# Kernel optimization log

Hardware: AMD Instinct MI355X
Metric: run time of the kernel (lower is better)

The kernel has to match this reference:

```python
import jax, jax.numpy as jnp
import numpy as np

DEPTH_BINS = 64
TEMPERATURE = 1.0


def _conv2d(x, w, b, pad):
    y = jax.lax.conv_general_dilated(x, w, (1, 1), [(pad, pad), (pad, pad)],
                                     dimension_numbers=('NCHW', 'OIHW', 'NCHW'))
    return y + b[None, :, None, None]


def _conv3d(x, w, b, pad):
    y = jax.lax.conv_general_dilated(x, w, (1, 1, 1), [(pad, pad)] * 3,
                                     dimension_numbers=('NCDHW', 'OIDHW', 'NCDHW'))
    return y + b[None, :, None, None, None]


def setup_inputs() -> dict:
    key = jax.random.key(0)
    ks = jax.random.split(key, 16)
    B, N, C, H, W = 2, 5, 256, 96, 96
    s = 0.05  # weight scale
    return {
        'focal_features': jax.random.normal(ks[0], (B, N, C, H, W), jnp.float32),
        'focus_distances': jax.random.uniform(ks[1], (B, N), jnp.float32, 0.5, 5.0),
        'camera_encoding': jax.random.normal(ks[2], (B, 16), jnp.float32),
        'W1': jax.random.normal(ks[3], (256, 512, 3, 3), jnp.float32) * s,
        'b1': jnp.zeros((256,), jnp.float32),
        'W2': jax.random.normal(ks[4], (128, 256, 3, 3), jnp.float32) * s,
        'b2': jnp.zeros((128,), jnp.float32),
        'W3': jax.random.normal(ks[5], (1, 128, 1, 1), jnp.float32) * s,
        'b3': jnp.zeros((1,), jnp.float32),
        'R1': jax.random.normal(ks[6], (32, 64, 3, 3, 3), jnp.float32) * s,
        'rb1': jnp.zeros((32,), jnp.float32),
        'R2': jax.random.normal(ks[7], (16, 32, 3, 3, 3), jnp.float32) * s,
        'rb2': jnp.zeros((16,), jnp.float32),
        'R3': jax.random.normal(ks[8], (64, 16, 1, 1, 1), jnp.float32) * s,
        'rb3': jnp.zeros((64,), jnp.float32),
    }


def reference(focal_features, focus_distances, camera_encoding,
              W1, b1, W2, b2, W3, b3, R1, rb1, R2, rb2, R3, rb3):
    B, N, C, H, W = focal_features.shape
    # _apply_blur is identity and depth only affects the (unused) blur sigma,
    # so the per-depth matching cost is identical across all depth bins.
    feat_ref = focal_features[:, 0]  # [B,C,H,W]
    pair = jnp.concatenate(
        [focal_features, jnp.broadcast_to(feat_ref[:, None], focal_features.shape)],
        axis=2)  # [B,N,2C,H,W]
    x = pair.reshape(B * N, 2 * C, H, W)
    x = jax.nn.relu(_conv2d(x, W1, b1, 1))
    x = jax.nn.relu(_conv2d(x, W2, b2, 1))
    cost = _conv2d(x, W3, b3, 0)  # [B*N,1,H,W]
    cost_agg = cost.reshape(B, N, H, W).mean(axis=1)  # [B,H,W]
    # identical for every depth bin -> broadcast
    cv = jnp.broadcast_to(cost_agg[:, None], (B, DEPTH_BINS, H, W))
    # refine_net: Conv3d over channels=depth_bins, spatial dims (H, W, 1)
    v = cv[..., None]  # [B, depth_bins, H, W, 1]
    v = jax.nn.relu(_conv3d(v, R1, rb1, 1))
    v = jax.nn.relu(_conv3d(v, R2, rb2, 1))
    v = _conv3d(v, R3, rb3, 0)  # [B, depth_bins, H, W, 1]
    cv_ref = v[..., 0]  # [B, depth_bins, H, W]
    depth_probs = jax.nn.softmax(-cv_ref / TEMPERATURE, axis=1)
    cost_volume = jnp.transpose(cv_ref, (0, 2, 3, 1))   # [B,H,W,depth_bins]
    depth_probs = jnp.transpose(depth_probs, (0, 2, 3, 1))
    return cost_volume, depth_probs
```

## Files before the change

kernel.cpp:

```cpp
#include <hip/hip_runtime.h>
#include <stdint.h>

typedef unsigned short u16;
typedef _Float16 f16;
typedef _Float16 f16x8 __attribute__((ext_vector_type(8)));
typedef float    f32x4 __attribute__((ext_vector_type(4)));

#define HW   96
#define NPIX (HW*HW)
#define BBATCH 2
#define NVIEW  5
#define NIMG 10

#define LDS_B_OFF 6272
#define LDS_BYTES (6272 + 24576)

__device__ __forceinline__ int swz(int row, int chunk) {
    return ((row >> 1) << 7) + (((((row & 1) << 2) | chunk) ^ ((row >> 1) & 7)) << 4);
}

__device__ __forceinline__ u16 f16u(float f) {
    union { u16 u; f16 h; } v; v.h = (f16)f; return v.u;
}

__global__ __launch_bounds__(256)
void k_prep_w(const float* __restrict__ W1, const float* __restrict__ W2,
              const float* __restrict__ R1, const float* __restrict__ R2, const float* __restrict__ R3,
              u16* __restrict__ w1a, u16* __restrict__ w1b, u16* __restrict__ w2t,
              float* __restrict__ s1t, float* __restrict__ s2t, float* __restrict__ r3t)
{
    int id = blockIdx.x * 256 + threadIdx.x;
    if (id < 589824) {
        int t = id >> 16; int r = id & 65535; int o = r >> 8; int c = r & 255;
        int kh = t / 3, kw = t % 3;
        *(f16*)&w1a[id] = (f16)W1[((size_t)(o * 512 + c) * 3 + kh) * 3 + kw];
        *(f16*)&w1b[id] = (f16)W1[((size_t)(o * 512 + 256 + c) * 3 + kh) * 3 + kw];
        return;
    }
    id -= 589824;
    if (id < 294912) {
        int t = id >> 15; int r = id & 32767; int o = r >> 8; int c = r & 255;
        *(f16*)&w2t[id] = (f16)W2[((size_t)(o * 256 + c) * 3 + t / 3) * 3 + (t % 3)];
        return;
    }
    id -= 294912;
    if (id < 288) {
        int t = id >> 5; int o = id & 31;
        float s = 0.f;
        for (int i = 0; i < 64; ++i)
            s += R1[((size_t)((o * 64 + i) * 3 + t / 3) * 3 + t % 3) * 3 + 1];
        s1t[id] = s;
        return;
    }
    id -= 288;
    if (id < 4608) {
        int o = id & 15; int r = id >> 4; int i = r & 31; int t = r >> 5;
        s2t[id] = R2[((size_t)((o * 32 + i) * 3 + t / 3) * 3 + t % 3) * 3 + 1];
        return;
    }
    id -= 4608;
    if (id < 1024) {
        int o = id & 63; int i = id >> 6;
        r3t[id] = R3[(size_t)o * 16 + i];
    }
}

__global__ __launch_bounds__(256)
void k_tr(const float* __restrict__ src, u16* __restrict__ dst, int img0, int imgMul)
{
    const int cblk = blockIdx.x, row = blockIdx.y, z = blockIdx.z;
    const int gimg = img0 + z * imgMul;
    const int tid = threadIdx.x;
    __shared__ u16 tile[96 * 40];
    const int c = tid >> 3, j = tid & 7;
    const float* s = src + ((size_t)(gimg * 256 + cblk * 32 + c)) * NPIX + (size_t)row * HW + j * 12;
    #pragma unroll
    for (int k = 0; k < 3; ++k) {
        const float4 v = ((const float4*)s)[k];
        const int px = j * 12 + k * 4;
        tile[(px + 0) * 40 + c] = f16u(v.x);
        tile[(px + 1) * 40 + c] = f16u(v.y);
        tile[(px + 2) * 40 + c] = f16u(v.z);
        tile[(px + 3) * 40 + c] = f16u(v.w);
    }
    __syncthreads();
    if (tid < 192) {
        const int px = tid >> 1, part = tid & 1;
        const uint4 v0 = ((const uint4*)(tile + px * 40 + part * 16))[0];
        const uint4 v1 = ((const uint4*)(tile + px * 40 + part * 16))[1];
        uint4* d = (uint4*)(dst + ((((size_t)z * HW + row) * 8 + cblk) * HW + px) * 32 + part * 16);
        d[0] = v0; d[1] = v1;
    }
}

template<int MODE>
__global__ __launch_bounds__(256, 4)
void k_conv(const u16* __restrict__ in, const u16* __restrict__ wt,
            const u16* __restrict__ refp, const float* __restrict__ bias,
            const float* __restrict__ W3, void* __restrict__ outp, int ib)
{
    constexpr int Cout = (MODE == 2) ? 128 : 256;
    const int h  = blockIdx.x;
    const int y  = blockIdx.y;
    const int ob = blockIdx.z * 128;
    const int tid = threadIdx.x;
    const int wv = tid >> 6, l = tid & 63;
    const int wm = wv >> 1, wn = wv & 1;
    const int lane16 = l & 15, quad = l >> 4;

    __shared__ __align__(16) char lds[LDS_BYTES];

    f32x4 acc[3][4];
    #pragma unroll
    for (int mf = 0; mf < 3; ++mf)
        #pragma unroll
        for (int nf = 0; nf < 4; ++nf) acc[mf][nf] = (f32x4){0.f, 0.f, 0.f, 0.f};

    if (tid < 32) {
        const int base = (tid & 16) ? (48 * 128 + 64) : 0;
        ((unsigned int*)(lds + base))[tid & 15] = 0u;
    }

    for (int dh = -1; dh <= 1; ++dh) {
        const int hh = h + dh;
        if ((unsigned)hh >= (unsigned)HW) continue;
        for (int c0 = 0; c0 < 256; c0 += 32) {
            __syncthreads();
            if (tid < 192) {
                const int px = tid >> 1, half = tid & 1;
                const uint4* g = (const uint4*)(in +
                    ((((size_t)y * HW + hh) * 8 + (c0 >> 5)) * HW + px) * 32 + half * 16);
                const uint4 v0 = g[0], v1 = g[1];
                *(uint4*)(lds + swz(px + 1, half * 2))     = v0;
                *(uint4*)(lds + swz(px + 1, half * 2 + 1)) = v1;
            }
            #pragma unroll
            for (int i = 0; i < 3; ++i) {
                const int idx = i * 256 + tid;
                const int dwt = idx >> 8, o = (idx >> 1) & 127, half = idx & 1;
                const int tap = (dh + 1) * 3 + dwt;
                const uint4* g = (const uint4*)(wt +
                    ((size_t)tap * Cout + ob + o) * 256 + c0 + half * 16);
                const uint4 v0 = g[0], v1 = g[1];
                const int row = dwt * 128 + o;
                *(uint4*)(lds + LDS_B_OFF + swz(row, half * 2))     = v0;
                *(uint4*)(lds + LDS_B_OFF + swz(row, half * 2 + 1)) = v1;
            }
            __syncthreads();
            #pragma unroll
            for (int dw = 0; dw < 3; ++dw) {
                f16x8 af[3];
                #pragma unroll
                for (int mf = 0; mf < 3; ++mf)
                    af[mf] = *(const f16x8*)(lds + swz(wm * 48 + mf * 16 + lane16 + dw, quad));
                #pragma unroll
                for (int nf = 0; nf < 4; ++nf) {
                    const f16x8 bf = *(const f16x8*)(lds + LDS_B_OFF +
                        swz(dw * 128 + wn * 64 + nf * 16 + lane16, quad));
                    #pragma unroll
                    for (int mf = 0; mf < 3; ++mf)
                        acc[mf][nf] = __builtin_amdgcn_mfma_f32_16x16x32_f16(af[mf], bf, acc[mf][nf], 0, 0, 0);
                }
            }
        }
    }

    if (MODE <= 1) {
        const int rimg = (MODE == 1) ? (ib + y) / NVIEW : 0;
        float bias4[4] = {0.f, 0.f, 0.f, 0.f};
        if (MODE == 1) {
            #pragma unroll
            for (int nf = 0; nf < 4; ++nf) bias4[nf] = bias[ob + wn * 64 + nf * 16 + lane16];
        }
        char* epi = lds + wv * 3072;
        u16* outg = (u16*)outp;
        #pragma unroll
        for (int p = 0; p < 2; ++p) {
            __syncthreads();
            #pragma unroll
            for (int nn = 0; nn < 2; ++nn) {
                const int nf = p * 2 + nn;
                #pragma unroll
                for (int mf = 0; mf < 3; ++mf)
                    #pragma unroll
                    for (int r = 0; r < 4; ++r) {
                        const int pxl = mf * 16 + quad * 4 + r;
                        *(u16*)(epi + pxl * 64 + (nn * 16 + lane16) * 2) =
                            f16u(acc[mf][nf][r] + bias4[nf]);
                    }
            }
            __syncthreads();
            const int cblk = (ob + wn * 64 + p * 32) >> 5;
            const size_t obase = (((size_t)y * HW + h) * 8 + cblk) * (size_t)(HW * 32);
            const size_t rbase = (((size_t)rimg * HW + h) * 8 + cblk) * (size_t)(HW * 32);
            #pragma unroll
            for (int i = 0; i < 3; ++i) {
                const int u = i * 64 + l;
                const int pxl = u >> 2, part = u & 3;
                f16x8 v = *(const f16x8*)(epi + pxl * 64 + part * 16);
                const int px = wm * 48 + pxl;
                if (MODE == 1) {
                    const f16x8 rv = *(const f16x8*)(refp + rbase + (size_t)px * 32 + part * 8);
                    #pragma unroll
                    for (int jj = 0; jj < 8; ++jj)
                        v[jj] = (f16)fmaxf((float)v[jj] + (float)rv[jj], 0.f);
                }
                *(f16x8*)(outg + obase + (size_t)px * 32 + part * 8) = v;
            }
        }
    } else {
        const int gimg = ib + y;
        float w3v[4], b2v[4];
        #pragma unroll
        for (int nf = 0; nf < 4; ++nf) {
            const int o = wn * 64 + nf * 16 + lane16;
            w3v[nf] = W3[o]; b2v[nf] = bias[o];
        }
        float s[3][4];
        #pragma unroll
        for (int mf = 0; mf < 3; ++mf)
            #pragma unroll
            for (int r = 0; r < 4; ++r) {
                float t = 0.f;
                #pragma unroll
                for (int nf = 0; nf < 4; ++nf)
                    t += w3v[nf] * fmaxf(acc[mf][nf][r] + b2v[nf], 0.f);
                s[mf][r] = t;
            }
        #pragma unroll
        for (int xb = 1; xb < 16; xb <<= 1)
            #pragma unroll
            for (int mf = 0; mf < 3; ++mf)
                #pragma unroll
                for (int r = 0; r < 4; ++r)
                    s[mf][r] += __shfl_xor(s[mf][r], xb);
        __syncthreads();
        float* cs = (float*)lds;
        if (wn == 0 && lane16 == 0) {
            #pragma unroll
            for (int mf = 0; mf < 3; ++mf)
                #pragma unroll
                for (int r = 0; r < 4; ++r)
                    cs[wm * 48 + mf * 16 + quad * 4 + r] = s[mf][r];
        }
        __syncthreads();
        if (wn == 1 && lane16 == 0) {
            float* pvp = (float*)outp + (size_t)gimg * NPIX + (size_t)h * HW;
            #pragma unroll
            for (int mf = 0; mf < 3; ++mf)
                #pragma unroll
                for (int r = 0; r < 4; ++r) {
                    const int px = wm * 48 + mf * 16 + quad * 4 + r;
                    pvp[px] = cs[px] + s[mf][r];
                }
        }
    }
}

__global__ __launch_bounds__(256)
void k_cost_sum(const float* __restrict__ pv, const float* __restrict__ b3, float* __restrict__ ca)
{
    const int id = blockIdx.x * 256 + threadIdx.x;
    if (id >= BBATCH * NPIX) return;
    const int b = id / NPIX, hw = id % NPIX;
    float s = 0.f;
    #pragma unroll
    for (int n = 0; n < NVIEW; ++n) s += pv[(size_t)(b * NVIEW + n) * NPIX + hw];
    ca[id] = b3[0] + 0.2f * s;
}

__global__ __launch_bounds__(256)
void k_d1(const float* __restrict__ cost_agg, const float* __restrict__ s1t,
          const float* __restrict__ rb1, float* __restrict__ t1)
{
    const int id = blockIdx.x * 256 + threadIdx.x;
    const int o = id & 31; const int r = id >> 5;
    const int hw = r % NPIX; const int bimg = r / NPIX;
    const int y = hw / HW, x = hw % HW;
    const float* ca = cost_agg + (size_t)bimg * NPIX;
    float s = rb1[o];
    #pragma unroll
    for (int t = 0; t < 9; ++t) {
        const int yy = y + t / 3 - 1, xx = x + t % 3 - 1;
        if ((unsigned)yy < HW && (unsigned)xx < HW)
            s += s1t[t * 32 + o] * ca[yy * HW + xx];
    }
    t1[id] = fmaxf(s, 0.f);
}

__global__ __launch_bounds__(256)
void k_d2(const float* __restrict__ t1, const float* __restrict__ s2t,
          const float* __restrict__ rb2, float* __restrict__ t2)
{
    const int id = blockIdx.x * 256 + threadIdx.x;
    const int o = id & 15; const int r = id >> 4;
    const int hw = r % NPIX; const int bimg = r / NPIX;
    const int y = hw / HW, x = hw % HW;
    float s = rb2[o];
    for (int t = 0; t < 9; ++t) {
        const int yy = y + t / 3 - 1, xx = x + t % 3 - 1;
        if ((unsigned)yy < HW && (unsigned)xx < HW) {
            const float* tp = t1 + ((size_t)bimg * NPIX + yy * HW + xx) * 32;
            #pragma unroll
            for (int i = 0; i < 32; ++i)
                s += s2t[(t * 32 + i) * 16 + o] * tp[i];
        }
    }
    t2[id] = fmaxf(s, 0.f);
}

__global__ __launch_bounds__(256)
void k_d3(const float* __restrict__ t2, const float* __restrict__ r3t,
          const float* __restrict__ rb3, float* __restrict__ out)
{
    const int wv = threadIdx.x >> 6, o = threadIdx.x & 63;
    const int pix = blockIdx.x * 4 + wv;
    const float* tp = t2 + (size_t)pix * 16;
    float cv = rb3[o];
    #pragma unroll
    for (int i = 0; i < 16; ++i) cv += r3t[i * 64 + o] * tp[i];
    const float z = -cv;
    float m = z;
    #pragma unroll
    for (int off = 32; off; off >>= 1) m = fmaxf(m, __shfl_xor(m, off));
    const float e = __expf(z - m);
    float s = e;
    #pragma unroll
    for (int off = 32; off; off >>= 1) s += __shfl_xor(s, off);
    const float p = e / s;
    const size_t idx = (size_t)pix * 64 + o;
    out[idx] = cv;
    out[idx + (size_t)BBATCH * NPIX * 64] = p;
}

extern "C" void kernel_launch(void* const* d_in, const int* in_sizes, int n_in,
                              void* d_out, int out_size, void* d_ws, size_t ws_size,
                              hipStream_t stream)
{
    (void)in_sizes; (void)n_in; (void)out_size;
    const float* focal = (const float*)d_in[0];
    const float* W1  = (const float*)d_in[3];
    const float* b1  = (const float*)d_in[4];
    const float* W2  = (const float*)d_in[5];
    const float* b2  = (const float*)d_in[6];
    const float* W3  = (const float*)d_in[7];
    const float* b3  = (const float*)d_in[8];
    const float* R1  = (const float*)d_in[9];
    const float* rb1 = (const float*)d_in[10];
    const float* R2  = (const float*)d_in[11];
    const float* rb2 = (const float*)d_in[12];
    const float* R3  = (const float*)d_in[13];
    const float* rb3 = (const float*)d_in[14];

    char* ws = (char*)d_ws;
    size_t off = 0;
    auto alloc = [&](size_t sz) { char* p = ws + off; off = (off + sz + 255) & ~(size_t)255; return p; };
    const size_t IMG = (size_t)HW * 8 * HW * 32 * 2;
    u16*   w1a  = (u16*)  alloc(1179648);
    u16*   w1b  = (u16*)  alloc(1179648);
    u16*   w2t  = (u16*)  alloc(589824);
    float* s1t  = (float*)alloc(1152);
    float* s2t  = (float*)alloc(18432);
    float* r3t  = (float*)alloc(4096);
    float* ca   = (float*)alloc(73728);
    float* t1   = (float*)alloc(2359296);
    float* t2   = (float*)alloc(1179648);
    float* pv   = (float*)alloc(NIMG * NPIX * 4);
    u16*   refp   = (u16*)alloc(BBATCH * IMG);
    u16*   feats2 = (u16*)alloc(BBATCH * IMG);
    const size_t base = off;
    int C = 1;
    if (base + 20 * IMG + 512 <= ws_size)      C = 10;
    else if (base + 10 * IMG + 512 <= ws_size) C = 5;
    else if (base + 4 * IMG + 512 <= ws_size)  C = 2;
    u16* feats = (u16*)alloc((size_t)C * IMG);
    u16* x1    = (u16*)alloc((size_t)C * IMG);

    k_prep_w<<<(890656 + 255) / 256, 256, 0, stream>>>(W1, W2, R1, R2, R3, w1a, w1b, w2t, s1t, s2t, r3t);

    k_tr<<<dim3(8, HW, BBATCH), 256, 0, stream>>>(focal, feats2, 0, NVIEW);
    k_conv<0><<<dim3(HW, BBATCH, 2), 256, 0, stream>>>(feats2, w1b, nullptr, nullptr, nullptr, refp, 0);

    for (int ib = 0; ib < NIMG; ib += C) {
        k_tr<<<dim3(8, HW, C), 256, 0, stream>>>(focal, feats, ib, 1);
        k_conv<1><<<dim3(HW, C, 2), 256, 0, stream>>>(feats, w1a, refp, b1, nullptr, x1, ib);
        k_conv<2><<<dim3(HW, C, 1), 256, 0, stream>>>(x1, w2t, nullptr, b2, W3, pv, ib);
    }

    k_cost_sum<<<(BBATCH * NPIX + 255) / 256, 256, 0, stream>>>(pv, b3, ca);
    k_d1<<<(BBATCH * NPIX * 32) / 256, 256, 0, stream>>>(ca, s1t, rb1, t1);
    k_d2<<<(BBATCH * NPIX * 16) / 256, 256, 0, stream>>>(t1, s2t, rb2, t2);
    k_d3<<<(BBATCH * NPIX) / 4, 256, 0, stream>>>(t2, r3t, rb3, (float*)d_out);
}
```

Measured before the change: 460.8 us.

## Load conv tiles directly into LDS with global_load_lds and repack weights

Replaces the register-staged global->LDS copies of activation and weight tiles with global_load_lds 16-byte direct transfers. Per-lane source offsets are precomputed so the existing XOR-swizzled LDS layout is kept. Weights are repacked into channel-block-major order so each 32-channel chunk is contiguous. The aim is to cut VGPR traffic and instruction overhead in the load phase. It relies on the async LDS writes being complete at the barrier, and correctness depends on the offset mapping matching the swizzle.

```diff
diff --git a/kernel.cpp b/kernel.cpp
--- a/kernel.cpp
+++ b/kernel.cpp
@@ -19,6 +19,12 @@
     return ((row >> 1) << 7) + (((((row & 1) << 2) | chunk) ^ ((row >> 1) & 7)) << 4);
 }
 
+__device__ __forceinline__ void gl16(const u16* g, char* l) {
+    __builtin_amdgcn_global_load_lds(
+        (const __attribute__((address_space(1))) void*)g,
+        (__attribute__((address_space(3))) void*)l, 16, 0, 0);
+}
+
 __device__ __forceinline__ u16 f16u(float f) {
     union { u16 u; f16 h; } v; v.h = (f16)f; return v.u;
 }
@@ -33,14 +39,16 @@
     if (id < 589824) {
         int t = id >> 16; int r = id & 65535; int o = r >> 8; int c = r & 255;
         int kh = t / 3, kw = t % 3;
-        *(f16*)&w1a[id] = (f16)W1[((size_t)(o * 512 + c) * 3 + kh) * 3 + kw];
-        *(f16*)&w1b[id] = (f16)W1[((size_t)(o * 512 + 256 + c) * 3 + kh) * 3 + kw];
+        const int dst = (((c >> 5) * 9 + t) * 256 + o) * 32 + (c & 31);
+        *(f16*)&w1a[dst] = (f16)W1[((size_t)(o * 512 + c) * 3 + kh) * 3 + kw];
+        *(f16*)&w1b[dst] = (f16)W1[((size_t)(o * 512 + 256 + c) * 3 + kh) * 3 + kw];
         return;
     }
     id -= 589824;
     if (id < 294912) {
         int t = id >> 15; int r = id & 32767; int o = r >> 8; int c = r & 255;
-        *(f16*)&w2t[id] = (f16)W2[((size_t)(o * 256 + c) * 3 + t / 3) * 3 + (t % 3)];
+        const int dst = (((c >> 5) * 9 + t) * 128 + o) * 32 + (c & 31);
+        *(f16*)&w2t[dst] = (f16)W2[((size_t)(o * 256 + c) * 3 + t / 3) * 3 + (t % 3)];
         return;
     }
     id -= 294912;
@@ -116,6 +124,30 @@
         #pragma unroll
         for (int nf = 0; nf < 4; ++nf) acc[mf][nf] = (f32x4){0.f, 0.f, 0.f, 0.f};
 
+    int aoff[2] = {0, 0};
+    #pragma unroll
+    for (int j = 0; j < 2; ++j) {
+        const int k = wv + 4 * j;
+        if (k < 6) {
+            const int t4 = 4 + l;
+            const int ln8 = t4 >> 3;
+            const int cpp = (t4 & 7) ^ (ln8 & 7);
+            const int row = 16 * k + 2 * ln8 + (cpp >> 2);
+            aoff[j] = (row - 1) * 32 + (cpp & 3) * 8;
+        }
+    }
+    int boff[6];
+    {
+        const int cpp = (l & 7) ^ (l >> 3);
+        #pragma unroll
+        for (int j = 0; j < 6; ++j) {
+            const int m = wv + 4 * j;
+            const int row = 16 * m + 2 * (l >> 3) + (cpp >> 2);
+            const int dwt = row >> 7, oo = row & 127;
+            boff[j] = (dwt * Cout + ob + oo) * 32 + (cpp & 3) * 8;
+        }
+    }
+
     if (tid < 32) {
         const int base = (tid & 16) ? (48 * 128 + 64) : 0;
         ((unsigned int*)(lds + base))[tid & 15] = 0u;
@@ -124,27 +156,20 @@
     for (int dh = -1; dh <= 1; ++dh) {
         const int hh = h + dh;
         if ((unsigned)hh >= (unsigned)HW) continue;
+        const int tb = (dh + 1) * 3;
         for (int c0 = 0; c0 < 256; c0 += 32) {
             __syncthreads();
-            if (tid < 192) {
-                const int px = tid >> 1, half = tid & 1;
-                const uint4* g = (const uint4*)(in +
-                    ((((size_t)y * HW + hh) * 8 + (c0 >> 5)) * HW + px) * 32 + half * 16);
-                const uint4 v0 = g[0], v1 = g[1];
-                *(uint4*)(lds + swz(px + 1, half * 2))     = v0;
-                *(uint4*)(lds + swz(px + 1, half * 2 + 1)) = v1;
-            }
-            #pragma unroll
-            for (int i = 0; i < 3; ++i) {
-                const int idx = i * 256 + tid;
-                const int dwt = idx >> 8, o = (idx >> 1) & 127, half = idx & 1;
-                const int tap = (dh + 1) * 3 + dwt;
-                const uint4* g = (const uint4*)(wt +
-                    ((size_t)tap * Cout + ob + o) * 256 + c0 + half * 16);
-                const uint4 v0 = g[0], v1 = g[1];
-                const int row = dwt * 128 + o;
-                *(uint4*)(lds + LDS_B_OFF + swz(row, half * 2))     = v0;
-                *(uint4*)(lds + LDS_B_OFF + swz(row, half * 2 + 1)) = v1;
+            {
+                const size_t abase = ((((size_t)y * HW + hh) * 8 + (c0 >> 5)) * (size_t)HW) * 32;
+                gl16(in + abase + aoff[0], lds + 64 + 1024 * wv);
+                if (wv < 2)
+                    gl16(in + abase + aoff[1], lds + 64 + 1024 * (wv + 4));
+            }
+            {
+                const size_t bbase = (size_t)((c0 >> 5) * 9 + tb) * Cout * 32;
+                #pragma unroll
+                for (int j = 0; j < 6; ++j)
+                    gl16(wt + bbase + boff[j], lds + LDS_B_OFF + 1024 * (wv + 4 * j));
             }
             __syncthreads();
             #pragma unroll
```

Measured after the change: 425.7 us. 7.6% less time.
